# Performance work log

Measured on AMD Instinct MI355X. Metric: run time of the kernel, lower is better.

## Reference

```python
import jax, jax.numpy as jnp
import numpy as np

S, B, L = 512, 256, 128  # seq_length, batch_size, label_nums
PAD_ID, START_ID = 0, 1


def setup_inputs() -> dict:
    key = jax.random.key(0)
    k1, k2, k3, k4 = jax.random.split(key, 4)
    emit_scores = jax.random.normal(k1, (S, B, L), dtype=jnp.float32)
    labels = jax.random.randint(k2, (B, S), 0, L, dtype=jnp.int32)
    # contiguous prefix masks: lengths in [1, S]
    lengths = jax.random.randint(k3, (B,), 1, S + 1, dtype=jnp.int32)
    masks = jnp.arange(S, dtype=jnp.int32)[None, :] < lengths[:, None]  # (B, S) bool
    T = jax.random.normal(k4, (L, L), dtype=jnp.float32) * 0.1  # transition params
    return {"emit_scores": emit_scores, "labels": labels, "masks": masks, "T": T}


def reference(emit_scores, labels, masks, T):
    seq_len, batch, label_nums = emit_scores.shape

    # ---- gold path score (calc_sentences_scores) ----
    lengths = masks.astype(jnp.int32).sum(axis=1)                       # (B,)
    ends_index = jnp.take_along_axis(labels, (lengths - 1)[:, None], axis=1)[:, 0]
    ends_scores = T[ends_index, PAD_ID].sum()

    labels_ext = jnp.concatenate(
        [jnp.full((batch, 1), START_ID, dtype=labels.dtype), labels], axis=1)  # (B, S+1)
    prev = labels_ext[:, :-1]                                           # (B, S)
    nxt = labels                                                        # (B, S)
    emit_bt = jnp.transpose(emit_scores, (1, 0, 2))                     # (B, S, L)
    emit_sel = jnp.take_along_axis(emit_bt, nxt[:, :, None], axis=2)[:, :, 0]  # (B, S)
    trans_sel = T[prev, nxt]                                            # (B, S)
    gold = jnp.where(masks, emit_sel + trans_sel, 0.0).sum() + ends_scores

    # ---- partition function (crf_encode): log-sum-exp scan over time ----
    fs0 = emit_scores[0] + T[START_ID][None, :]                         # (B, L)

    def step(fs, inp):
        e_t, m_t = inp                                                  # (B, L), (B,)
        # scores[b, i, j] = fs[b, i] + T[i, j] + e_t[b, j]
        scores = fs[:, :, None] + T[None, :, :] + e_t[:, None, :]
        cur = jax.nn.logsumexp(scores, axis=1)                          # (B, L)
        fs = jnp.where(m_t[:, None], cur, fs)
        return fs, None

    fs, _ = jax.lax.scan(step, fs0, (emit_scores[1:], masks.T[1:]))
    encode = jax.nn.logsumexp(fs + T[:, PAD_ID][None, :], axis=1).sum()

    return encode - gold
```

## Files before the change

kernel.cpp:

```cpp
#include <hip/hip_runtime.h>
#include <hip/hip_fp8.h>

#define S_LEN 512
#define BATCH 256
#define L 128
#define PAD_ID 0
#define START_ID 1

typedef int    i32x8 __attribute__((ext_vector_type(8)));
typedef int    i32x4 __attribute__((ext_vector_type(4)));
typedef float  f32x4 __attribute__((ext_vector_type(4)));
typedef unsigned int   u32x4 __attribute__((ext_vector_type(4)));
typedef unsigned short u16x2 __attribute__((ext_vector_type(2)));

__device__ __forceinline__ unsigned int umax2(unsigned int a, unsigned int b) {
    u16x2 x = __builtin_bit_cast(u16x2, a), y = __builtin_bit_cast(u16x2, b);
#if defined(__has_builtin) && __has_builtin(__builtin_elementwise_max)
    return __builtin_bit_cast(unsigned int, __builtin_elementwise_max(x, y));
#else
    u16x2 r; r.x = x.x > y.x ? x.x : y.x; r.y = x.y > y.y ? x.y : y.y;
    return __builtin_bit_cast(unsigned int, r);
#endif
}
__device__ __forceinline__ float frcp(float x) {
#if defined(__has_builtin) && __has_builtin(__builtin_amdgcn_rcpf)
    return __builtin_amdgcn_rcpf(x);
#else
    return 1.0f / x;
#endif
}
__device__ __forceinline__ unsigned short f2bf(float f) {
    unsigned int u = __builtin_bit_cast(unsigned int, f);
    return (unsigned short)((u + 0x7fffu + ((u >> 16) & 1u)) >> 16);
}
__device__ __forceinline__ float bf2f(unsigned short b) {
    return __builtin_bit_cast(float, (unsigned int)b << 16);
}
__device__ __forceinline__ float sane(float x, float lo, float hi) {
    return fminf(fmaxf(x, lo), hi);
}
__device__ __forceinline__ int pk2_fp8(float a, float b) {
#if defined(__has_builtin) && __has_builtin(__builtin_amdgcn_cvt_pk_fp8_f32)
    return __builtin_amdgcn_cvt_pk_fp8_f32(a, b, 0, false);
#else
    __hip_fp8_e4m3 A(a), B(b);
    return (int)A.__x | ((int)B.__x << 8);
#endif
}
__device__ __forceinline__ unsigned int bmax8(u32x4 a, u32x4 b) {
    const unsigned int M = 0x00FF00FFu;
    unsigned int l0 = umax2(a.x & M, a.y & M), l1 = umax2(a.z & M, a.w & M);
    unsigned int l2 = umax2(b.x & M, b.y & M), l3 = umax2(b.z & M, b.w & M);
    unsigned int h0 = umax2((a.x >> 8) & M, (a.y >> 8) & M);
    unsigned int h1 = umax2((a.z >> 8) & M, (a.w >> 8) & M);
    unsigned int h2 = umax2((b.x >> 8) & M, (b.y >> 8) & M);
    unsigned int h3 = umax2((b.z >> 8) & M, (b.w >> 8) & M);
    unsigned int v = umax2(umax2(umax2(l0, l1), umax2(l2, l3)),
                           umax2(umax2(h0, h1), umax2(h2, h3)));
    u16x2 t = __builtin_bit_cast(u16x2, v);
    return (unsigned int)(t.x > t.y ? t.x : t.y);
}
__device__ __forceinline__ float fp8dec(unsigned int bb) {
    bb &= 0x7Fu;
    int e = (int)(bb >> 3), mt = (int)(bb & 7u);
    float v = e ? __builtin_ldexpf((float)(8 + mt), e - 10)
                : __builtin_ldexpf((float)mt, -9);
    return sane(v, 1e-9f, 448.f);
}

#define WS_QF 0
#define WS_QB 32768
#define WS_SF 65536
#define WS_SB 66560
#define WS_N  67584

__global__ __launch_bounds__(256, 1) void k_scan2(
        const float* __restrict__ emit, const int* __restrict__ labels,
        const void* __restrict__ masks, const float* __restrict__ T,
        unsigned char* __restrict__ ws, float* __restrict__ out) {
    const int b   = blockIdx.x & (BATCH - 1);
    const int dir = blockIdx.x >> 8;
    const int tid = threadIdx.x;
    const int w = tid >> 6;
    const int lane = tid & 63;
    const int g = lane >> 4, m = lane & 15;
    const int ja = 32 * w + m, jb = ja + 16;

    __shared__ unsigned short elds[255][L];
    __shared__ __align__(16) unsigned char qs[2][L];
    __shared__ __align__(8)  unsigned char hb[2][4];
    __shared__ float part[4];
    __shared__ float fsx[4];
    __shared__ int   ib[4];

    {
        const unsigned int* mw0 = (const unsigned int*)masks;
        int pred = 0;
        #pragma unroll
        for (int k = 0; k < 8; ++k) {
            unsigned int w0 = mw0[tid + 256 * k];
            pred |= (w0 > 1u && w0 != 0x3f800000u);
        }
        unsigned long long bal = __ballot(pred);
        if (lane == 0) ib[w] = (bal != 0ull) ? 1 : 0;
        if (tid < 8)   ((unsigned char*)hb)[tid] = 0x38;
        if (tid < 256) ((unsigned char*)qs)[tid] = 0x38;
        if (tid < 4)   { part[tid] = 0.f; fsx[tid] = 0.f; }
    }
    __syncthreads();
    const bool isbyte = (ib[0] | ib[1] | ib[2] | ib[3]) != 0;

    int len;
    {
        int cnt = 0;
        if (isbyte) {
            const unsigned int* mw = (const unsigned int*)masks + b * (S_LEN / 4);
            #pragma unroll
            for (int k = 0; k < 2; ++k) {
                unsigned int w0 = mw[lane + 64 * k];
                cnt += ((w0 & 0xffu) != 0) + ((w0 & 0xff00u) != 0) +
                       ((w0 & 0xff0000u) != 0) + ((w0 & 0xff000000u) != 0);
            }
        } else {
            const unsigned int* mw = (const unsigned int*)masks + b * S_LEN;
            #pragma unroll
            for (int k = 0; k < 8; ++k) cnt += (mw[lane + 64 * k] != 0u);
        }
        #pragma unroll
        for (int off = 32; off; off >>= 1) cnt += __shfl_xor(cnt, off, 64);
        len = cnt;
    }
    const int n  = len - 1;
    const int kf = n / 2;
    const int nB = n - kf - 1;
    const int steps = dir ? (nB > 0 ? nB : 0) : kf;

#define LDBX(BF, nt, TR)                                                                     \
    {                                                                                        \
        _Pragma("unroll")                                                                    \
        for (int d = 0; d < 8; ++d) {                                                        \
            int s0 = 32 * g + 4 * d;                                                         \
            float v0, v1, v2, v3;                                                            \
            if (TR) {                                                                        \
                v0 = __expf(T[(16 * (nt) + m) * L + (16 * ((s0 + 0) & 7) + ((s0 + 0) >> 3))]); \
                v1 = __expf(T[(16 * (nt) + m) * L + (16 * ((s0 + 1) & 7) + ((s0 + 1) >> 3))]); \
                v2 = __expf(T[(16 * (nt) + m) * L + (16 * ((s0 + 2) & 7) + ((s0 + 2) >> 3))]); \
                v3 = __expf(T[(16 * (nt) + m) * L + (16 * ((s0 + 3) & 7) + ((s0 + 3) >> 3))]); \
            } else {                                                                         \
                v0 = __expf(T[(16 * ((s0 + 0) & 7) + ((s0 + 0) >> 3)) * L + 16 * (nt) + m]);   \
                v1 = __expf(T[(16 * ((s0 + 1) & 7) + ((s0 + 1) >> 3)) * L + 16 * (nt) + m]);   \
                v2 = __expf(T[(16 * ((s0 + 2) & 7) + ((s0 + 2) >> 3)) * L + 16 * (nt) + m]);   \
                v3 = __expf(T[(16 * ((s0 + 3) & 7) + ((s0 + 3) >> 3)) * L + 16 * (nt) + m]);   \
            }                                                                                \
            int p01 = pk2_fp8(v0, v1), p23 = pk2_fp8(v2, v3);                                \
            BF[d] = (p01 & 0xffff) | (p23 << 16);                                            \
        }                                                                                    \
    }
    i32x8 Bq0, Bq1;
    if (dir == 0) { LDBX(Bq0, 2 * w, 0) LDBX(Bq1, 2 * w + 1, 0) }
    else          { LDBX(Bq0, 2 * w, 1) LDBX(Bq1, 2 * w + 1, 1) }

    for (int idx = tid; idx < steps * 64; idx += 256) {
        int rl = idx >> 6, c2 = (idx & 63) * 2;
        int row = dir ? (kf + 1 + rl) : (1 + rl);
        const float* ep = emit + ((size_t)row * BATCH + b) * L + c2;
        float e0 = ep[0], e1 = ep[1];
        *(unsigned int*)&elds[rl][c2] =
            (unsigned int)f2bf(e0) | ((unsigned int)f2bf(e1) << 16);
    }

    float fa = 0.f, fbv = 0.f;
    const bool active = (dir == 0) || (n >= 1);
    if (dir == 0) {
        fa  = emit[b * L + ja] + T[START_ID * L + ja];
        fbv = emit[b * L + jb] + T[START_ID * L + jb];
    } else if (n >= 1) {
        fa  = emit[((size_t)n * BATCH + b) * L + ja] + T[ja * L + PAD_ID];
        fbv = emit[((size_t)n * BATCH + b) * L + jb] + T[jb * L + PAD_ID];
    }
    {
        float mx = fmaxf(fa, fbv);
        #pragma unroll
        for (int off = 32; off; off >>= 1) mx = fmaxf(mx, __shfl_xor(mx, off, 64));
        if (lane == 0) fsx[w] = mx;
    }
    __syncthreads();
    float S = 0.f, p0 = 0.f, p1 = 0.f;
    if (active) {
        S = fmaxf(fmaxf(fsx[0], fsx[1]), fmaxf(fsx[2], fsx[3]));
        p0 = sane(__expf(fa - S), 1e-9f, 400.f);
        p1 = sane(__expf(fbv - S), 1e-9f, 400.f);
        if (g == 0)
            *(short*)&qs[0][8 * m + 2 * w] = (short)(pk2_fp8(p0, p1) & 0xffff);
    }
    __syncthreads();

    const f32x4 z = {0.f, 0.f, 0.f, 0.f};
    for (int i = 0; i < steps; ++i) {
        const int rb = i & 1, wb2 = (i + 1) & 1;
        const int slot = dir ? (nB - 1 - i) : i;

        i32x4 alo = *(const i32x4*)&qs[rb][32 * g];
        i32x4 ahi = *(const i32x4*)&qs[rb][32 * g + 16];
        unsigned int hd = *(const unsigned int*)&hb[rb][0];
        float ea = bf2f(elds[slot][ja]);
        float eb = bf2f(elds[slot][jb]);
        float xe0 = __expf(ea), xe1 = __expf(eb);

        {
            const unsigned int M = 0x00FF00FFu;
            unsigned int v = umax2(hd & M, (hd >> 8) & M);
            u16x2 tv = __builtin_bit_cast(u16x2, v);
            hd = (unsigned int)(tv.x > tv.y ? tv.x : tv.y);
        }
        float msc = fp8dec(hd);
        float kk = frcp(msc);

        i32x8 A;
        A[0] = alo[0]; A[1] = alo[1]; A[2] = alo[2]; A[3] = alo[3];
        A[4] = ahi[0]; A[5] = ahi[1]; A[6] = ahi[2]; A[7] = ahi[3];

        f32x4 c0 = __builtin_amdgcn_mfma_scale_f32_16x16x128_f8f6f4(A, Bq0, z, 0, 0, 0, 127, 0, 127);
        f32x4 c1 = __builtin_amdgcn_mfma_scale_f32_16x16x128_f8f6f4(A, Bq1, z, 0, 0, 0, 127, 0, 127);

        unsigned int qm = bmax8(__builtin_bit_cast(u32x4, alo),
                                __builtin_bit_cast(u32x4, ahi));
        if (w == 0 && m == 0) hb[wb2][g] = (unsigned char)(qm & 0x7Fu);

        p0 = sane(c0[0] * kk * xe0, 1e-9f, 400.f);
        p1 = sane(c1[0] * kk * xe1, 1e-9f, 400.f);
        if (g == 0)
            *(short*)&qs[wb2][8 * m + 2 * w] = (short)(pk2_fp8(p0, p1) & 0xffff);
        S += __logf(msc);
        __syncthreads();
    }

    unsigned char* seam = ws + (dir ? WS_QB : WS_QF) + b * L;
    if (tid < 32) ((int*)seam)[tid] = ((const int*)qs[steps & 1])[tid];
    if (tid == 0) {
        ((float*)(ws + (dir ? WS_SB : WS_SF)))[b] = S;
        if (dir == 0) ((int*)(ws + WS_N))[b] = n;
    }

    if (dir == 0) {
        float gsum = 0.f;
        for (int tt = tid; tt < len; tt += 256) {
            int nxt = labels[b * S_LEN + tt];
            int prv = tt ? labels[b * S_LEN + tt - 1] : START_ID;
            gsum += emit[((size_t)tt * BATCH + b) * L + nxt] + T[prv * L + nxt];
            if (tt == len - 1) gsum += T[nxt * L + PAD_ID];
        }
        #pragma unroll
        for (int off = 32; off; off >>= 1) gsum += __shfl_xor(gsum, off, 64);
        if (lane == 0) part[w] = gsum;
        __syncthreads();
        if (tid == 0)
            atomicAdd(out, -((part[0] + part[1]) + (part[2] + part[3])));
    }
}

__global__ __launch_bounds__(64, 1) void k_join(
        const float* __restrict__ T, const unsigned char* __restrict__ ws,
        float* __restrict__ out) {
    const int b = blockIdx.x;
    const int lane = threadIdx.x;
    __shared__ float qsh[L], ush[L];

    const int n = ((const int*)(ws + WS_N))[b];
    #pragma unroll
    for (int k = 0; k < 2; ++k) {
        int s = lane + 64 * k;
        int j = 16 * (s & 7) + (s >> 3);
        qsh[j] = fp8dec(ws[WS_QF + b * L + s]);
        ush[j] = fp8dec(ws[WS_QB + b * L + s]);
    }
    __syncthreads();

    float ev = 0.f;
    if (n >= 1) {
        #pragma unroll
        for (int k = 0; k < 2; ++k) {
            int j = lane + 64 * k;
            float v = 0.f;
            for (int i = 0; i < L; ++i)
                v = fmaf(qsh[i], __expf(T[i * L + j]), v);
            ev += v * ush[j];
        }
    } else {
        #pragma unroll
        for (int k = 0; k < 2; ++k) {
            int j = lane + 64 * k;
            ev += qsh[j] * __expf(T[j * L + PAD_ID]);
        }
    }
    #pragma unroll
    for (int off = 32; off; off >>= 1) ev += __shfl_xor(ev, off, 64);

    if (lane == 0) {
        float Sf = ((const float*)(ws + WS_SF))[b];
        float Sb = (n >= 1) ? ((const float*)(ws + WS_SB))[b] : 0.f;
        float enc = Sf + Sb + __logf(fmaxf(ev, 1e-35f));
        atomicAdd(out, sane(enc, -1e30f, 1e30f));
    }
}

extern "C" void kernel_launch(void* const* d_in, const int* in_sizes, int n_in,
                              void* d_out, int out_size, void* d_ws, size_t ws_size,
                              hipStream_t stream) {
    const float* emit   = (const float*)d_in[0];
    const int*   labels = (const int*)d_in[1];
    const void*  masks  = d_in[2];
    const float* T      = (const float*)d_in[3];
    float* out = (float*)d_out;
    unsigned char* ws = (unsigned char*)d_ws;

    hipMemsetAsync(d_out, 0, sizeof(float), stream);
    k_scan2<<<dim3(2 * BATCH), dim3(256), 0, stream>>>(emit, labels, masks, T, ws, out);
    k_join <<<dim3(BATCH),     dim3(64),  0, stream>>>(T, ws, out);
}
```

Before: 227.9 us.

## Fuse join step into scan kernel using last-arriver atomics and MFMA

Removes the separate join kernel: each batch's forward/backward scan blocks count arrivals with an atomic, and the second block to finish combines both seams by reusing its in-register MFMA operands instead of a scalar 128x128 exp loop. A global done counter lets the final block reduce per-batch results deterministically into the output, replacing the atomicAdd on out and the memset of out. This removes one kernel launch and the join's redundant exp work, at the cost of threadfences, atomics and a small serial tail in the last block.

```diff
diff --git a/kernel.cpp b/kernel.cpp
--- a/kernel.cpp
+++ b/kernel.cpp
@@ -68,13 +68,16 @@
     return sane(v, 1e-9f, 448.f);
 }
 
-#define WS_QF 0
-#define WS_QB 32768
-#define WS_SF 65536
-#define WS_SB 66560
-#define WS_N  67584
-
-__global__ __launch_bounds__(256, 1) void k_scan2(
+#define WS_QF   0
+#define WS_QB   32768
+#define WS_SF   65536
+#define WS_SB   66560
+#define WS_G    67584
+#define WS_RES  68608
+#define WS_CNT  69632
+#define WS_DONE 70656
+
+__global__ __launch_bounds__(256, 1) void k_scan3(
         const float* __restrict__ emit, const int* __restrict__ labels,
         const void* __restrict__ masks, const float* __restrict__ T,
         unsigned char* __restrict__ ws, float* __restrict__ out) {
@@ -92,6 +95,7 @@
     __shared__ float part[4];
     __shared__ float fsx[4];
     __shared__ int   ib[4];
+    __shared__ int   arriv;
 
     {
         const unsigned int* mw0 = (const unsigned int*)masks;
@@ -237,11 +241,9 @@
 
     unsigned char* seam = ws + (dir ? WS_QB : WS_QF) + b * L;
     if (tid < 32) ((int*)seam)[tid] = ((const int*)qs[steps & 1])[tid];
-    if (tid == 0) {
-        ((float*)(ws + (dir ? WS_SB : WS_SF)))[b] = S;
-        if (dir == 0) ((int*)(ws + WS_N))[b] = n;
-    }
-
+    if (tid == 0) ((float*)(ws + (dir ? WS_SB : WS_SF)))[b] = S;
+
+    float gold = 0.f;
     if (dir == 0) {
         float gsum = 0.f;
         for (int tt = tid; tt < len; tt += 256) {
@@ -254,53 +256,64 @@
         for (int off = 32; off; off >>= 1) gsum += __shfl_xor(gsum, off, 64);
         if (lane == 0) part[w] = gsum;
         __syncthreads();
-        if (tid == 0)
-            atomicAdd(out, -((part[0] + part[1]) + (part[2] + part[3])));
-    }
-}
-
-__global__ __launch_bounds__(64, 1) void k_join(
-        const float* __restrict__ T, const unsigned char* __restrict__ ws,
-        float* __restrict__ out) {
-    const int b = blockIdx.x;
-    const int lane = threadIdx.x;
-    __shared__ float qsh[L], ush[L];
-
-    const int n = ((const int*)(ws + WS_N))[b];
-    #pragma unroll
-    for (int k = 0; k < 2; ++k) {
-        int s = lane + 64 * k;
-        int j = 16 * (s & 7) + (s >> 3);
-        qsh[j] = fp8dec(ws[WS_QF + b * L + s]);
-        ush[j] = fp8dec(ws[WS_QB + b * L + s]);
-    }
-    __syncthreads();
-
+        gold = (part[0] + part[1]) + (part[2] + part[3]);
+        if (tid == 0) ((float*)(ws + WS_G))[b] = gold;
+    }
+
+    __threadfence();
+    if (tid == 0) arriv = atomicAdd((int*)(ws + WS_CNT) + b, 1);
+    __syncthreads();
+    if (arriv != 1) return;
+
+    __threadfence();
     float ev = 0.f;
     if (n >= 1) {
-        #pragma unroll
-        for (int k = 0; k < 2; ++k) {
-            int j = lane + 64 * k;
-            float v = 0.f;
-            for (int i = 0; i < L; ++i)
-                v = fmaf(qsh[i], __expf(T[i * L + j]), v);
-            ev += v * ush[j];
+        const unsigned char* oseam = ws + (dir ? WS_QF : WS_QB) + b * L;
+        i32x4 alo = *(const i32x4*)&qs[steps & 1][32 * g];
+        i32x4 ahi = *(const i32x4*)&qs[steps & 1][32 * g + 16];
+        i32x8 A;
+        A[0] = alo[0]; A[1] = alo[1]; A[2] = alo[2]; A[3] = alo[3];
+        A[4] = ahi[0]; A[5] = ahi[1]; A[6] = ahi[2]; A[7] = ahi[3];
+        f32x4 c0 = __builtin_amdgcn_mfma_scale_f32_16x16x128_f8f6f4(A, Bq0, z, 0, 0, 0, 127, 0, 127);
+        f32x4 c1 = __builtin_amdgcn_mfma_scale_f32_16x16x128_f8f6f4(A, Bq1, z, 0, 0, 0, 127, 0, 127);
+        if (g == 0) {
+            float o0 = fp8dec(oseam[8 * m + 2 * w]);
+            float o1 = fp8dec(oseam[8 * m + 2 * w + 1]);
+            ev = sane(c0[0], 0.f, 3e7f) * o0 + sane(c1[0], 0.f, 3e7f) * o1;
         }
     } else {
-        #pragma unroll
-        for (int k = 0; k < 2; ++k) {
-            int j = lane + 64 * k;
-            ev += qsh[j] * __expf(T[j * L + PAD_ID]);
+        if (g == 0) {
+            float q0 = (dir == 0) ? p0 : fp8dec(ws[WS_QF + b * L + 8 * m + 2 * w]);
+            float q1 = (dir == 0) ? p1 : fp8dec(ws[WS_QF + b * L + 8 * m + 2 * w + 1]);
+            ev = q0 * __expf(T[ja * L + PAD_ID]) + q1 * __expf(T[jb * L + PAD_ID]);
         }
     }
     #pragma unroll
     for (int off = 32; off; off >>= 1) ev += __shfl_xor(ev, off, 64);
-
-    if (lane == 0) {
-        float Sf = ((const float*)(ws + WS_SF))[b];
-        float Sb = (n >= 1) ? ((const float*)(ws + WS_SB))[b] : 0.f;
-        float enc = Sf + Sb + __logf(fmaxf(ev, 1e-35f));
-        atomicAdd(out, sane(enc, -1e30f, 1e30f));
+    if (lane == 0) part[w] = ev;
+    __syncthreads();
+    float evtot = fmaxf((part[0] + part[1]) + (part[2] + part[3]), 1e-35f);
+
+    float Sf = ((const float*)(ws + WS_SF))[b];
+    float Sb = (n >= 1) ? ((const float*)(ws + WS_SB))[b] : 0.f;
+    float enc = Sf + Sb + __logf(evtot);
+    if (dir == 1) gold = ((const float*)(ws + WS_G))[b];
+
+    if (tid == 0) {
+        ((float*)(ws + WS_RES))[b] = sane(enc - gold, -1e30f, 1e30f);
+        __threadfence();
+        arriv = atomicAdd((int*)(ws + WS_DONE), 1);
+    }
+    __syncthreads();
+    if (arriv == BATCH - 1) {
+        __threadfence();
+        if (tid < 64) {
+            const float* res = (const float*)(ws + WS_RES);
+            float s = (res[tid] + res[tid + 64]) + (res[tid + 128] + res[tid + 192]);
+            #pragma unroll
+            for (int off = 32; off; off >>= 1) s += __shfl_xor(s, off, 64);
+            if (tid == 0) out[0] = s;
+        }
     }
 }
 
@@ -314,7 +327,6 @@
     float* out = (float*)d_out;
     unsigned char* ws = (unsigned char*)d_ws;
 
-    hipMemsetAsync(d_out, 0, sizeof(float), stream);
-    k_scan2<<<dim3(2 * BATCH), dim3(256), 0, stream>>>(emit, labels, masks, T, ws, out);
-    k_join <<<dim3(BATCH),     dim3(64),  0, stream>>>(T, ws, out);
-}
+    hipMemsetAsync(ws + WS_CNT, 0, 2048, stream);
+    k_scan3<<<dim3(2 * BATCH), dim3(256), 0, stream>>>(emit, labels, masks, T, ws, out);
+}
```

Result: no change. 228.3 us (+0.2%).
